# Kernel tuning notes

Hardware: AMD Instinct MI355X
Metric: run time of the kernel (lower is better)

Reference implementation:

```python
import jax, jax.numpy as jnp
import numpy as np

N_NODES = 50000
N_EDGES = 1600000
N_GRAPHS = 64
DIM_IN, DIM_H, HEADS, DIM_OUT = 128, 32, 2, 64
NEG_SLOPE = 0.2


def _segment_softmax(scores, seg, num_segments):
    # scores: [E, H], seg: [E] int -> softmax over edges sharing the same dst
    m = jax.ops.segment_max(scores, seg, num_segments=num_segments)
    m = jnp.where(jnp.isfinite(m), m, 0.0)  # empty segments -> -inf; neutralize
    e = jnp.exp(scores - m[seg])
    s = jax.ops.segment_sum(e, seg, num_segments=num_segments)
    return e / (s[seg] + 1e-16)


def gatv2_conv(x, edge_index, Wl, Wr, att, bias, heads, ch, n_nodes):
    # PyG GATv2Conv defaults: add_self_loops=True, share_weights=False, concat heads.
    loops = jnp.arange(n_nodes, dtype=edge_index.dtype)
    ei = jnp.concatenate([edge_index, jnp.stack([loops, loops])], axis=1)
    src, dst = ei[0], ei[1]
    xl = (x @ Wl).reshape(n_nodes, heads, ch)  # source transform
    xr = (x @ Wr).reshape(n_nodes, heads, ch)  # target transform
    el = xl[src]                               # [E+N, H, C] gather
    s = jax.nn.leaky_relu(el + xr[dst], NEG_SLOPE)
    scores = jnp.einsum('ehc,hc->eh', s, att)  # [E+N, H]
    alpha = _segment_softmax(scores, dst, n_nodes)
    out = jax.ops.segment_sum(alpha[..., None] * el, dst, num_segments=n_nodes)
    return out.reshape(n_nodes, heads * ch) + bias


def setup_inputs() -> dict:
    key = jax.random.key(0)
    ks = jax.random.split(key, 12)
    glorot = lambda k, shp: jax.random.normal(k, shp, jnp.float32) * np.sqrt(2.0 / (shp[0] + shp[-1]))
    x = jax.random.normal(ks[0], (N_NODES, DIM_IN), jnp.float32)
    edge_index = jax.random.randint(ks[1], (2, N_EDGES), 0, N_NODES, jnp.int64)
    batch = jnp.sort(jax.random.randint(ks[2], (N_NODES,), 0, N_GRAPHS, jnp.int64))
    H1 = DIM_H * HEADS
    return {
        'x': x, 'edge_index': edge_index, 'batch': batch,
        'Wl1': glorot(ks[3], (DIM_IN, H1)), 'Wr1': glorot(ks[4], (DIM_IN, H1)),
        'att1': glorot(ks[5], (HEADS, DIM_H)), 'b1': jnp.zeros((H1,), jnp.float32),
        'Wl2': glorot(ks[6], (H1, DIM_OUT)), 'Wr2': glorot(ks[7], (H1, DIM_OUT)),
        'att2': glorot(ks[8], (1, DIM_OUT)), 'b2': jnp.zeros((DIM_OUT,), jnp.float32),
        'lin_w': glorot(ks[9], (DIM_OUT, 2)), 'lin_b': jnp.zeros((2,), jnp.float32),
    }


def reference(x, edge_index, batch, Wl1, Wr1, att1, b1, Wl2, Wr2, att2, b2, lin_w, lin_b):
    # eval mode: dropout is identity
    h = gatv2_conv(x, edge_index, Wl1, Wr1, att1, b1, HEADS, DIM_H, N_NODES)
    h = jax.nn.elu(h)
    h = jax.nn.elu(gatv2_conv(h, edge_index, Wl2, Wr2, att2, b2, 1, DIM_OUT, N_NODES))
    # global mean pool over graphs
    sums = jax.ops.segment_sum(h, batch, num_segments=N_GRAPHS)
    cnts = jax.ops.segment_sum(jnp.ones((N_NODES,), h.dtype), batch, num_segments=N_GRAPHS)
    pooled = sums / jnp.maximum(cnts, 1.0)[:, None]
    return pooled @ lin_w + lin_b
```

## Files before the change

kernel.cpp:

```cpp
#include <hip/hip_runtime.h>
#include <hip/hip_bf16.h>
#include <math.h>

#define N_NODES 50000
#define N_EDGES 1600000
#define N_GRAPHS 64
#define NB 391
#define NBLK 256
#define CHUNK 6250
#define ROW_STRIDE 80
#define SENT 50047

typedef unsigned int u32;

__device__ __forceinline__ float bcf(u32 u) { return __builtin_bit_cast(float, u); }

template <int CTRL>
__device__ __forceinline__ float dpp_add(float v) {
    int r = __builtin_amdgcn_update_dpp(0, __builtin_bit_cast(int, v), CTRL, 0xF, 0xF, true);
    return v + __builtin_bit_cast(float, r);
}

__device__ __forceinline__ u32 pack_bf16x2(float lo, float hi) {
    unsigned short l = __builtin_bit_cast(unsigned short, __float2bfloat16(lo));
    unsigned short h = __builtin_bit_cast(unsigned short, __float2bfloat16(hi));
    return (u32)l | ((u32)h << 16);
}

__global__ __launch_bounds__(256) void count_kernel(
    const int* __restrict__ ei, int* __restrict__ countsRM) {
    __shared__ int h[NB];
    const int t = threadIdx.x;
    for (int k = t; k < NB; k += 256) h[k] = 0;
    __syncthreads();
    const int base = blockIdx.x * CHUNK;
    for (int e = base + t; e < base + CHUNK; e += 256)
        atomicAdd(&h[ei[N_EDGES + e] >> 7], 1);
    __syncthreads();
    for (int k = t; k < NB; k += 256) countsRM[blockIdx.x * NB + k] = h[k];
}

__global__ __launch_bounds__(256) void scan_bucket(
    const int* __restrict__ countsRM, int* __restrict__ scanT,
    int* __restrict__ totals) {
    __shared__ int tmp[256];
    const int b = blockIdx.x;
    const int t = threadIdx.x;
    const int v0 = countsRM[t * NB + b];
    tmp[t] = v0;
    __syncthreads();
    for (int off = 1; off < 256; off <<= 1) {
        int v = (t >= off) ? tmp[t - off] : 0;
        __syncthreads();
        tmp[t] += v;
        __syncthreads();
    }
    scanT[b * 256 + t] = tmp[t] - v0;
    if (t == 255) totals[b] = tmp[t];
}

__global__ __launch_bounds__(512) void scan_total(
    const int* __restrict__ totals, int* __restrict__ bucketBase,
    float* __restrict__ alb) {
    __shared__ int tmp[512];
    const int t = threadIdx.x;
    const int v0 = (t < NB) ? totals[t] : 0;
    tmp[t] = v0;
    __syncthreads();
    for (int off = 1; off < 512; off <<= 1) {
        int v = (t >= off) ? tmp[t - off] : 0;
        __syncthreads();
        tmp[t] += v;
        __syncthreads();
    }
    if (t < NB) bucketBase[t] = tmp[t] - v0;
    if (t == NB - 1) bucketBase[NB] = tmp[t];
    if (t == 0) { alb[(size_t)SENT * 2] = -1e30f; alb[(size_t)SENT * 2 + 1] = -1e30f; }
}

template <int K, bool FUSE_SCATTER>
__global__ __launch_bounds__(256) void gemm_tiled(
    const float* __restrict__ x, const float* __restrict__ Wl,
    const float* __restrict__ Wr, const float* __restrict__ att,
    u32* __restrict__ xlb, float* __restrict__ xr,
    float* __restrict__ alb, float* __restrict__ arb,
    const int* __restrict__ ei, const int* __restrict__ scanT,
    const int* __restrict__ bb, int* __restrict__ sortedE, int gemmBlocks) {
    __shared__ float xs[64][65];
    __shared__ float als[64];
    const int t = threadIdx.x;
    if (FUSE_SCATTER && blockIdx.x >= gemmBlocks) {
        int* cursor = (int*)&xs[0][0];
        const int b = blockIdx.x - gemmBlocks;
        for (int k = t; k < NB; k += 256)
            cursor[k] = bb[k] + scanT[k * 256 + b];
        __syncthreads();
        const int base = b * CHUNK;
        for (int e = base + t; e < base + CHUNK; e += 256) {
            const int s = ei[e];
            const int d = ei[N_EDGES + e];
            const int idx = atomicAdd(&cursor[d >> 7], 1);
            sortedE[idx] = (s << 7) | (d & 127);
        }
        return;
    }
    const int base = blockIdx.x * 64;
    const int lane = t & 63;
    const int w = __builtin_amdgcn_readfirstlane(t >> 6);
    const float* __restrict__ W = (w < 2) ? Wl : Wr;
    const int cb = (w & 1) * 32;
    float acc[32];
#pragma unroll
    for (int j = 0; j < 32; ++j) acc[j] = 0.f;
#pragma unroll
    for (int c = 0; c < K / 64; ++c) {
        if (c) __syncthreads();
        for (int f = t; f < 1024; f += 256) {
            const int row = f >> 4;
            const int c4 = f & 15;
            float4 v = make_float4(0.f, 0.f, 0.f, 0.f);
            if (base + row < N_NODES)
                v = *(const float4*)(x + (size_t)(base + row) * K + c * 64 + c4 * 4);
            xs[row][c4 * 4 + 0] = v.x;
            xs[row][c4 * 4 + 1] = v.y;
            xs[row][c4 * 4 + 2] = v.z;
            xs[row][c4 * 4 + 3] = v.w;
        }
        __syncthreads();
#pragma unroll 2
        for (int kk = 0; kk < 64; ++kk) {
            const float xv = xs[lane][kk];
            const float* __restrict__ Wrow = W + (c * 64 + kk) * 64 + cb;
#pragma unroll
            for (int j = 0; j < 32; ++j) acc[j] = fmaf(xv, Wrow[j], acc[j]);
        }
    }
    const int n = base + lane;
    float av = 0.f;
#pragma unroll
    for (int j = 0; j < 32; ++j) av = fmaf(att[cb + j], acc[j], av);
    if (K == 64) {
        if (w == 0) als[lane] = av;
        __syncthreads();
        if (w == 1 && n < N_NODES) alb[n] = als[lane] + av;
        if (blockIdx.x == 0 && t == 0) alb[SENT] = -1e30f;
    } else {
        if (w < 2 && n < N_NODES) alb[(size_t)n * 2 + (w & 1)] = av;
    }
    if (n < N_NODES) {
        if (w < 2) {
            u32 pk[16];
#pragma unroll
            for (int j = 0; j < 32; j += 2) pk[j >> 1] = pack_bf16x2(acc[j], acc[j + 1]);
            uint4* dst = (uint4*)(xlb + (size_t)n * 32 + (w & 1) * 16);
#pragma unroll
            for (int j = 0; j < 4; ++j)
                dst[j] = make_uint4(pk[j * 4], pk[j * 4 + 1], pk[j * 4 + 2], pk[j * 4 + 3]);
        } else {
            arb[(size_t)n * 2 + (w & 1)] = av;
#pragma unroll
            for (int j = 0; j < 32; j += 4) {
                float4 v = {acc[j], acc[j + 1], acc[j + 2], acc[j + 3]};
                *(float4*)(xr + (size_t)n * 64 + cb + j) = v;
            }
        }
    }
}

__global__ __launch_bounds__(256) void expand_kernel(
    const int* __restrict__ bucketBase, const int* __restrict__ sortedE,
    int* __restrict__ deg, int* __restrict__ rows) {
    __shared__ int ldeg[128];
    const int b = blockIdx.x;
    const int t = threadIdx.x;
    const int node_base = b * 128;
    if (t < 128) {
        const int n = node_base + t;
        ldeg[t] = 1;
        if (n < N_NODES) rows[(size_t)n * ROW_STRIDE] = n;
    }
    __syncthreads();
    const int beg = bucketBase[b];
    const int end = bucketBase[b + 1];
    for (int i = beg + t; i < end; i += 256) {
        const int en = sortedE[i];
        const int ld = en & 127;
        const int pos = atomicAdd(&ldeg[ld], 1);
        if (pos < ROW_STRIDE) rows[(size_t)(node_base + ld) * ROW_STRIDE + pos] = en >> 7;
    }
    __syncthreads();
    if (t < 128) {
        const int n = node_base + t;
        if (n < N_NODES) {
            int c = ldeg[t];
            c = c < ROW_STRIDE ? c : ROW_STRIDE;
            const int cp = (c + 7) & ~7;
            for (int j = c; j < cp; ++j) rows[(size_t)n * ROW_STRIDE + j] = SENT;
            deg[n] = cp;
        }
    }
}

template <bool L1>
__global__ __launch_bounds__(256) void node_layer(
    const int* __restrict__ deg, const int* __restrict__ rows,
    const u32* __restrict__ xlb, const float* __restrict__ xr,
    const float* __restrict__ alb, const float* __restrict__ arb,
    const float* __restrict__ att, const float* __restrict__ bias,
    float* __restrict__ hout) {
    const int n = (blockIdx.x * 256 + threadIdx.x) >> 6;
    const int lane = threadIdx.x & 63;
    const int sub = lane & 7;
    const int g = lane >> 3;
    const float4 xra = *(const float4*)(xr + (size_t)n * 64 + sub * 8);
    const float4 xrb = *(const float4*)(xr + (size_t)n * 64 + sub * 8 + 4);
    const float4 ata = *(const float4*)(att + sub * 8);
    const float4 atb = *(const float4*)(att + sub * 8 + 4);
    const float2 ar2 = *(const float2*)(arb + (size_t)n * 2);
    const float based = 0.6f * (L1 ? ((sub & 4) ? ar2.y : ar2.x) : (ar2.x + ar2.y));

    float c0 = 0.f, c1 = 0.f, c2 = 0.f, c3 = 0.f;
    float c4 = 0.f, c5 = 0.f, c6 = 0.f, c7 = 0.f;
    float ssum = 0.f;
    const int cp = __builtin_amdgcn_readfirstlane(deg[n]);
    const int* __restrict__ row = rows + (size_t)n * ROW_STRIDE;
    for (int i = 0; i < cp; i += 8) {
        const int s = row[i + g];
        const float als = L1 ? alb[(size_t)s * 2 + ((sub >> 2) & 1)] : alb[s];
        const uint4 r4 = *(const uint4*)(xlb + (size_t)s * 32 + sub * 4);
        const float a0 = bcf(r4.x << 16), a1 = bcf(r4.x & 0xFFFF0000u);
        const float a2f = bcf(r4.y << 16), a3 = bcf(r4.y & 0xFFFF0000u);
        const float a4 = bcf(r4.z << 16), a5 = bcf(r4.z & 0xFFFF0000u);
        const float a6 = bcf(r4.w << 16), a7 = bcf(r4.w & 0xFFFF0000u);
        float v = ata.x * fabsf(a0 + xra.x);
        v = fmaf(ata.y, fabsf(a1 + xra.y), v);
        v = fmaf(ata.z, fabsf(a2f + xra.z), v);
        v = fmaf(ata.w, fabsf(a3 + xra.w), v);
        v = fmaf(atb.x, fabsf(a4 + xrb.x), v);
        v = fmaf(atb.y, fabsf(a5 + xrb.y), v);
        v = fmaf(atb.z, fabsf(a6 + xrb.z), v);
        v = fmaf(atb.w, fabsf(a7 + xrb.w), v);
        v = dpp_add<0xB1>(v);
        v = dpp_add<0x4E>(v);
        if (!L1) v = dpp_add<0x141>(v);
        const float ev = __expf(fmaf(0.6f, als, fmaf(0.4f, v, based)));
        c0 = fmaf(ev, a0, c0); c1 = fmaf(ev, a1, c1);
        c2 = fmaf(ev, a2f, c2); c3 = fmaf(ev, a3, c3);
        c4 = fmaf(ev, a4, c4); c5 = fmaf(ev, a5, c5);
        c6 = fmaf(ev, a6, c6); c7 = fmaf(ev, a7, c7);
        ssum += ev;
    }
#define XRED(x) x += __shfl_xor(x, 8); x += __shfl_xor(x, 16); x += __shfl_xor(x, 32);
    XRED(c0) XRED(c1) XRED(c2) XRED(c3) XRED(c4) XRED(c5) XRED(c6) XRED(c7) XRED(ssum)
#undef XRED
    if (g == 0) {
        const float inv = 1.f / (ssum + 1e-16f);
        const float4 ba = *(const float4*)(bias + sub * 8);
        const float4 bb = *(const float4*)(bias + sub * 8 + 4);
        float o[8] = {c0 * inv + ba.x, c1 * inv + ba.y, c2 * inv + ba.z, c3 * inv + ba.w,
                      c4 * inv + bb.x, c5 * inv + bb.y, c6 * inv + bb.z, c7 * inv + bb.w};
#pragma unroll
        for (int j = 0; j < 8; ++j) o[j] = o[j] > 0.f ? o[j] : expm1f(o[j]);
        *(float4*)(hout + (size_t)n * 64 + sub * 8) = make_float4(o[0], o[1], o[2], o[3]);
        *(float4*)(hout + (size_t)n * 64 + sub * 8 + 4) = make_float4(o[4], o[5], o[6], o[7]);
    }
}

__global__ __launch_bounds__(64) void pool_kernel(
    const float* __restrict__ h2, const int* __restrict__ batch,
    float* __restrict__ pooled, float* __restrict__ cnt) {
    const int t = threadIdx.x;
    const int base = blockIdx.x * 64;
    float local = 0.f, lc = 0.f;
    int cur = -1;
    for (int j = 0; j < 64; ++j) {
        const int n = base + j;
        if (n >= N_NODES) break;
        const int g = batch[n];
        if (g != cur) {
            if (cur >= 0) {
                unsafeAtomicAdd(&pooled[cur * 64 + t], local);
                if (t == 0) unsafeAtomicAdd(&cnt[cur], lc);
            }
            cur = g; local = 0.f; lc = 0.f;
        }
        local += h2[n * 64 + t];
        lc += 1.f;
    }
    if (cur >= 0) {
        unsafeAtomicAdd(&pooled[cur * 64 + t], local);
        if (t == 0) unsafeAtomicAdd(&cnt[cur], lc);
    }
}

__global__ __launch_bounds__(128) void head_kernel(
    const float* __restrict__ pooled, const float* __restrict__ cnt,
    const float* __restrict__ lin_w, const float* __restrict__ lin_b,
    float* __restrict__ out) {
    const int i = threadIdx.x;
    const int g = i >> 1, k = i & 1;
    float c = cnt[g];
    c = c > 1.f ? c : 1.f;
    float a = 0.f;
#pragma unroll
    for (int j = 0; j < 64; ++j) a = fmaf(pooled[g * 64 + j] / c, lin_w[j * 2 + k], a);
    out[i] = a + lin_b[k];
}

extern "C" void kernel_launch(void* const* d_in, const int* in_sizes, int n_in,
                              void* d_out, int out_size, void* d_ws, size_t ws_size,
                              hipStream_t stream) {
    const float* x     = (const float*)d_in[0];
    const int*   ei    = (const int*)d_in[1];
    const int*   batch = (const int*)d_in[2];
    const float* Wl1   = (const float*)d_in[3];
    const float* Wr1   = (const float*)d_in[4];
    const float* att1  = (const float*)d_in[5];
    const float* b1    = (const float*)d_in[6];
    const float* Wl2   = (const float*)d_in[7];
    const float* Wr2   = (const float*)d_in[8];
    const float* att2  = (const float*)d_in[9];
    const float* b2    = (const float*)d_in[10];
    const float* lin_w = (const float*)d_in[11];
    const float* lin_b = (const float*)d_in[12];

    float* ws = (float*)d_ws;
    u32*   xlb      = (u32*)ws;
    float* xr       = ws + 1601536;
    float* h1       = ws + 4801536;
    float* alb      = ws + 8001536;
    float* arb      = ws + 8101632;
    int*   rows     = (int*)(ws + 8201728);
    int*   deg      = (int*)(ws + 12205568);
    int*   countsRM = (int*)(ws + 12255616);
    int*   scanT    = (int*)(ws + 12355712);
    int*   totals   = (int*)(ws + 12455808);
    int*   bb       = (int*)(ws + 12456320);
    float* pooled   = ws + 12456832;
    float* cnt      = ws + 12460928;
    int*   sortedE  = (int*)(ws + 12460992);

    hipMemsetAsync(pooled, 0, (size_t)(4096 + 64) * sizeof(float), stream);

    const int gblocks = (N_NODES + 63) / 64;

    count_kernel<<<NBLK, 256, 0, stream>>>(ei, countsRM);
    scan_bucket<<<NB, 256, 0, stream>>>(countsRM, scanT, totals);
    scan_total<<<1, 512, 0, stream>>>(totals, bb, alb);

    gemm_tiled<128, true><<<gblocks + NBLK, 256, 0, stream>>>(
        x, Wl1, Wr1, att1, xlb, xr, alb, arb, ei, scanT, bb, sortedE, gblocks);

    expand_kernel<<<NB, 256, 0, stream>>>(bb, sortedE, deg, rows);

    node_layer<true><<<N_NODES / 4, 256, 0, stream>>>(
        deg, rows, xlb, xr, alb, arb, att1, b1, h1);

    gemm_tiled<64, false><<<gblocks, 256, 0, stream>>>(
        h1, Wl2, Wr2, att2, xlb, xr, alb, arb, nullptr, nullptr, nullptr, nullptr, gblocks);
    node_layer<false><<<N_NODES / 4, 256, 0, stream>>>(
        deg, rows, xlb, xr, alb, arb, att2, b2, h1);

    pool_kernel<<<(N_NODES + 63) / 64, 64, 0, stream>>>(h1, batch, pooled, cnt);
    head_kernel<<<1, 128, 0, stream>>>(pooled, cnt, lin_w, lin_b, (float*)d_out);
}
```

Baseline: 302.8 us.

## Replace scalar FMA GEMMs with bf16 MFMA using split hi/lo weights

Both node-transform GEMMs now use 16x16x32 bf16 MFMA instructions instead of per-thread scalar FMAs. Inputs are pre-converted to bf16 (x in a kernel fused with edge counting, h1 written directly as bf16 by layer 1). Weights are packed into MFMA fragment layout as hi plus lo bf16 parts to keep accuracy close to fp32 on the weight side. The output goes through a shared-memory transpose so the attention dot products and stores can be computed per node. This adds small conversion kernels and introduces bf16 rounding of the activations.

Measured after the change: 297.8 us. Within noise of the previous version (-1.6%).

```diff
diff --git a/kernel.cpp b/kernel.cpp
--- a/kernel.cpp
+++ b/kernel.cpp
@@ -12,6 +12,8 @@
 #define SENT 50047
 
 typedef unsigned int u32;
+typedef __attribute__((ext_vector_type(8))) __bf16 bf16x8;
+typedef __attribute__((ext_vector_type(4))) float f32x4;
 
 __device__ __forceinline__ float bcf(u32 u) { return __builtin_bit_cast(float, u); }
 
@@ -27,17 +29,61 @@
     return (u32)l | ((u32)h << 16);
 }
 
-__global__ __launch_bounds__(256) void count_kernel(
-    const int* __restrict__ ei, int* __restrict__ countsRM) {
+template <int K>
+__global__ __launch_bounds__(256) void conv_w(
+    const float* __restrict__ Wl, const float* __restrict__ Wr,
+    u32* __restrict__ wfHi, u32* __restrict__ wfLo) {
+    const int KO = K / 32;
+    for (int idx = threadIdx.x; idx < KO * 8 * 64; idx += 256) {
+        const int L = idx & 63;
+        const int tile = idx >> 6;
+        const int ko = tile >> 3, nt = tile & 7;
+        const int c = nt * 16 + (L & 15);
+        u32 hi[4], lo[4];
+        float hv[8], lv[8];
+#pragma unroll
+        for (int i = 0; i < 8; ++i) {
+            const int k = ko * 32 + (L >> 4) * 8 + i;
+            const float wv = (c < 64) ? Wl[k * 64 + c] : Wr[k * 64 + (c - 64)];
+            const __hip_bfloat16 h = __float2bfloat16(wv);
+            hv[i] = wv;
+            lv[i] = wv - __bfloat162float(h);
+        }
+#pragma unroll
+        for (int i = 0; i < 4; ++i) {
+            hi[i] = pack_bf16x2(hv[2 * i], hv[2 * i + 1]);
+            lo[i] = pack_bf16x2(lv[2 * i], lv[2 * i + 1]);
+        }
+        *(uint4*)(wfHi + (size_t)idx * 4) = make_uint4(hi[0], hi[1], hi[2], hi[3]);
+        *(uint4*)(wfLo + (size_t)idx * 4) = make_uint4(lo[0], lo[1], lo[2], lo[3]);
+    }
+}
+
+__global__ __launch_bounds__(256) void conv_x_count(
+    const float* __restrict__ x, u32* __restrict__ xbf,
+    const int* __restrict__ ei, int* __restrict__ countsRM, int convBlocks) {
     __shared__ int h[NB];
-    const int t = threadIdx.x;
-    for (int k = t; k < NB; k += 256) h[k] = 0;
-    __syncthreads();
-    const int base = blockIdx.x * CHUNK;
-    for (int e = base + t; e < base + CHUNK; e += 256)
-        atomicAdd(&h[ei[N_EDGES + e] >> 7], 1);
-    __syncthreads();
-    for (int k = t; k < NB; k += 256) countsRM[blockIdx.x * NB + k] = h[k];
+    if (blockIdx.x >= convBlocks) {
+        const int t = threadIdx.x;
+        const int cb = blockIdx.x - convBlocks;
+        for (int k = t; k < NB; k += 256) h[k] = 0;
+        __syncthreads();
+        const int base = cb * CHUNK;
+        for (int e = base + t; e < base + CHUNK; e += 256)
+            atomicAdd(&h[ei[N_EDGES + e] >> 7], 1);
+        __syncthreads();
+        for (int k = t; k < NB; k += 256) countsRM[cb * NB + k] = h[k];
+        return;
+    }
+    const int units = N_NODES * 128 / 8;
+    const int stride = convBlocks * 256;
+    for (int u = blockIdx.x * 256 + threadIdx.x; u < units; u += stride) {
+        const float4 a = *(const float4*)(x + (size_t)u * 8);
+        const float4 b = *(const float4*)(x + (size_t)u * 8 + 4);
+        *(uint4*)(xbf + (size_t)u * 4) = make_uint4(
+            pack_bf16x2(a.x, a.y), pack_bf16x2(a.z, a.w),
+            pack_bf16x2(b.x, b.y), pack_bf16x2(b.z, b.w));
+    }
 }
 
 __global__ __launch_bounds__(256) void scan_bucket(
@@ -79,18 +125,18 @@
 }
 
 template <int K, bool FUSE_SCATTER>
-__global__ __launch_bounds__(256) void gemm_tiled(
-    const float* __restrict__ x, const float* __restrict__ Wl,
-    const float* __restrict__ Wr, const float* __restrict__ att,
+__global__ __launch_bounds__(256) void gemm_mfma(
+    const u32* __restrict__ xbf, const u32* __restrict__ wfHi,
+    const u32* __restrict__ wfLo, const float* __restrict__ att,
     u32* __restrict__ xlb, float* __restrict__ xr,
     float* __restrict__ alb, float* __restrict__ arb,
     const int* __restrict__ ei, const int* __restrict__ scanT,
     const int* __restrict__ bb, int* __restrict__ sortedE, int gemmBlocks) {
-    __shared__ float xs[64][65];
-    __shared__ float als[64];
+    __shared__ float Ct[64][129];
+    __shared__ float alq[64][4];
     const int t = threadIdx.x;
     if (FUSE_SCATTER && blockIdx.x >= gemmBlocks) {
-        int* cursor = (int*)&xs[0][0];
+        int* cursor = (int*)&Ct[0][0];
         const int b = blockIdx.x - gemmBlocks;
         for (int k = t; k < NB; k += 256)
             cursor[k] = bb[k] + scanT[k * 256 + b];
@@ -104,67 +150,91 @@
         }
         return;
     }
-    const int base = blockIdx.x * 64;
+    const int KO = K / 32;
     const int lane = t & 63;
     const int w = __builtin_amdgcn_readfirstlane(t >> 6);
-    const float* __restrict__ W = (w < 2) ? Wl : Wr;
-    const int cb = (w & 1) * 32;
-    float acc[32];
-#pragma unroll
-    for (int j = 0; j < 32; ++j) acc[j] = 0.f;
-#pragma unroll
-    for (int c = 0; c < K / 64; ++c) {
-        if (c) __syncthreads();
-        for (int f = t; f < 1024; f += 256) {
-            const int row = f >> 4;
-            const int c4 = f & 15;
-            float4 v = make_float4(0.f, 0.f, 0.f, 0.f);
-            if (base + row < N_NODES)
-                v = *(const float4*)(x + (size_t)(base + row) * K + c * 64 + c4 * 4);
-            xs[row][c4 * 4 + 0] = v.x;
-            xs[row][c4 * 4 + 1] = v.y;
-            xs[row][c4 * 4 + 2] = v.z;
-            xs[row][c4 * 4 + 3] = v.w;
-        }
-        __syncthreads();
-#pragma unroll 2
-        for (int kk = 0; kk < 64; ++kk) {
-            const float xv = xs[lane][kk];
-            const float* __restrict__ Wrow = W + (c * 64 + kk) * 64 + cb;
-#pragma unroll
-            for (int j = 0; j < 32; ++j) acc[j] = fmaf(xv, Wrow[j], acc[j]);
-        }
-    }
-    const int n = base + lane;
+    const int quad = lane >> 4;
+    const int m16 = lane & 15;
+    const int base = blockIdx.x * 64;
+    const int arow = base + w * 16 + m16;
+    const u32* aptr = xbf + ((size_t)arow * K + quad * 8) / 2;
+
+    f32x4 acc[8];
+    const f32x4 zz = {0.f, 0.f, 0.f, 0.f};
+#pragma unroll
+    for (int i = 0; i < 8; ++i) acc[i] = zz;
+
+#pragma unroll
+    for (int ko = 0; ko < KO; ++ko) {
+        const uint4 au = *(const uint4*)(aptr + ko * 16);
+        const bf16x8 af = __builtin_bit_cast(bf16x8, au);
+#pragma unroll
+        for (int nt = 0; nt < 8; ++nt) {
+            const uint4 bh = *(const uint4*)(wfHi + (size_t)((ko * 8 + nt) * 64 + lane) * 4);
+            acc[nt] = __builtin_amdgcn_mfma_f32_16x16x32_bf16(
+                af, __builtin_bit_cast(bf16x8, bh), acc[nt], 0, 0, 0);
+        }
+#pragma unroll
+        for (int nt = 0; nt < 8; ++nt) {
+            const uint4 bl = *(const uint4*)(wfLo + (size_t)((ko * 8 + nt) * 64 + lane) * 4);
+            acc[nt] = __builtin_amdgcn_mfma_f32_16x16x32_bf16(
+                af, __builtin_bit_cast(bf16x8, bl), acc[nt], 0, 0, 0);
+        }
+    }
+#pragma unroll
+    for (int nt = 0; nt < 8; ++nt)
+#pragma unroll
+        for (int r = 0; r < 4; ++r)
+            Ct[w * 16 + quad * 4 + r][nt * 16 + m16] = acc[nt][r];
+    __syncthreads();
+
+    const int node = t & 63;
+    const int q = t >> 6;
+    const int n = base + node;
     float av = 0.f;
-#pragma unroll
-    for (int j = 0; j < 32; ++j) av = fmaf(att[cb + j], acc[j], av);
-    if (K == 64) {
-        if (w == 0) als[lane] = av;
-        __syncthreads();
-        if (w == 1 && n < N_NODES) alb[n] = als[lane] + av;
-        if (blockIdx.x == 0 && t == 0) alb[SENT] = -1e30f;
-    } else {
-        if (w < 2 && n < N_NODES) alb[(size_t)n * 2 + (w & 1)] = av;
-    }
     if (n < N_NODES) {
-        if (w < 2) {
+        if (q < 2) {
             u32 pk[16];
 #pragma unroll
-            for (int j = 0; j < 32; j += 2) pk[j >> 1] = pack_bf16x2(acc[j], acc[j + 1]);
-            uint4* dst = (uint4*)(xlb + (size_t)n * 32 + (w & 1) * 16);
+            for (int j = 0; j < 32; j += 2) {
+                const float v0 = Ct[node][q * 32 + j];
+                const float v1 = Ct[node][q * 32 + j + 1];
+                av = fmaf(att[q * 32 + j], v0, av);
+                av = fmaf(att[q * 32 + j + 1], v1, av);
+                pk[j >> 1] = pack_bf16x2(v0, v1);
+            }
+            uint4* dst = (uint4*)(xlb + (size_t)n * 32 + q * 16);
 #pragma unroll
             for (int j = 0; j < 4; ++j)
                 dst[j] = make_uint4(pk[j * 4], pk[j * 4 + 1], pk[j * 4 + 2], pk[j * 4 + 3]);
         } else {
-            arb[(size_t)n * 2 + (w & 1)] = av;
+            const int cb = (q - 2) * 32;
 #pragma unroll
             for (int j = 0; j < 32; j += 4) {
-                float4 v = {acc[j], acc[j + 1], acc[j + 2], acc[j + 3]};
+                float4 v = {Ct[node][64 + cb + j], Ct[node][64 + cb + j + 1],
+                            Ct[node][64 + cb + j + 2], Ct[node][64 + cb + j + 3]};
+                av = fmaf(att[cb + j], v.x, av);
+                av = fmaf(att[cb + j + 1], v.y, av);
+                av = fmaf(att[cb + j + 2], v.z, av);
+                av = fmaf(att[cb + j + 3], v.w, av);
                 *(float4*)(xr + (size_t)n * 64 + cb + j) = v;
             }
         }
     }
+    alq[node][q] = av;
+    __syncthreads();
+    if (t < 64 && base + t < N_NODES) {
+        const int nn = base + t;
+        if (K == 128) {
+            alb[(size_t)nn * 2] = alq[t][0];
+            alb[(size_t)nn * 2 + 1] = alq[t][1];
+        } else {
+            alb[nn] = alq[t][0] + alq[t][1];
+        }
+        arb[(size_t)nn * 2] = alq[t][2];
+        arb[(size_t)nn * 2 + 1] = alq[t][3];
+    }
+    if (K == 64 && blockIdx.x == 0 && t == 0) alb[SENT] = -1e30f;
 }
 
 __global__ __launch_bounds__(256) void expand_kernel(
@@ -207,7 +277,7 @@
     const u32* __restrict__ xlb, const float* __restrict__ xr,
     const float* __restrict__ alb, const float* __restrict__ arb,
     const float* __restrict__ att, const float* __restrict__ bias,
-    float* __restrict__ hout) {
+    u32* __restrict__ houtB, float* __restrict__ houtF) {
     const int n = (blockIdx.x * 256 + threadIdx.x) >> 6;
     const int lane = threadIdx.x & 63;
     const int sub = lane & 7;
@@ -261,8 +331,14 @@
                       c4 * inv + bb.x, c5 * inv + bb.y, c6 * inv + bb.z, c7 * inv + bb.w};
 #pragma unroll
         for (int j = 0; j < 8; ++j) o[j] = o[j] > 0.f ? o[j] : expm1f(o[j]);
-        *(float4*)(hout + (size_t)n * 64 + sub * 8) = make_float4(o[0], o[1], o[2], o[3]);
-        *(float4*)(hout + (size_t)n * 64 + sub * 8 + 4) = make_float4(o[4], o[5], o[6], o[7]);
+        if (L1) {
+            *(uint4*)(houtB + (size_t)n * 32 + sub * 4) = make_uint4(
+                pack_bf16x2(o[0], o[1]), pack_bf16x2(o[2], o[3]),
+                pack_bf16x2(o[4], o[5]), pack_bf16x2(o[6], o[7]));
+        } else {
+            *(float4*)(houtF + (size_t)n * 64 + sub * 8) = make_float4(o[0], o[1], o[2], o[3]);
+            *(float4*)(houtF + (size_t)n * 64 + sub * 8 + 4) = make_float4(o[4], o[5], o[6], o[7]);
+        }
     }
 }
 
@@ -325,42 +401,52 @@
     const float* lin_b = (const float*)d_in[12];
 
     float* ws = (float*)d_ws;
-    u32*   xlb      = (u32*)ws;
-    float* xr       = ws + 1601536;
-    float* h1       = ws + 4801536;
-    float* alb      = ws + 8001536;
-    float* arb      = ws + 8101632;
-    int*   rows     = (int*)(ws + 8201728);
-    int*   deg      = (int*)(ws + 12205568);
-    int*   countsRM = (int*)(ws + 12255616);
-    int*   scanT    = (int*)(ws + 12355712);
-    int*   totals   = (int*)(ws + 12455808);
-    int*   bb       = (int*)(ws + 12456320);
-    float* pooled   = ws + 12456832;
-    float* cnt      = ws + 12460928;
-    int*   sortedE  = (int*)(ws + 12460992);
+    u32*   xbf      = (u32*)ws;
+    u32*   h1b      = (u32*)(ws + 3203072);
+    u32*   xlb      = (u32*)(ws + 4804608);
+    float* xr       = ws + 6406144;
+    float* h2       = ws + 9609216;
+    float* alb      = ws + 12812288;
+    float* arb      = ws + 12912384;
+    int*   rows     = (int*)(ws + 13012480);
+    int*   deg      = (int*)(ws + 17016320);
+    int*   countsRM = (int*)(ws + 17066368);
+    int*   scanT    = (int*)(ws + 17166464);
+    int*   totals   = (int*)(ws + 17266560);
+    int*   bb       = (int*)(ws + 17267072);
+    float* pooled   = ws + 17267584;
+    float* cnt      = ws + 17271680;
+    int*   sortedE  = (int*)(ws + 17271744);
+    u32*   wf1hi    = (u32*)(ws + 18871744);
+    u32*   wf1lo    = (u32*)(ws + 18879936);
+    u32*   wf2hi    = (u32*)(ws + 18888128);
+    u32*   wf2lo    = (u32*)(ws + 18892224);
 
     hipMemsetAsync(pooled, 0, (size_t)(4096 + 64) * sizeof(float), stream);
 
     const int gblocks = (N_NODES + 63) / 64;
-
-    count_kernel<<<NBLK, 256, 0, stream>>>(ei, countsRM);
+    const int convBlocks = 512;
+
+    conv_w<128><<<1, 256, 0, stream>>>(Wl1, Wr1, wf1hi, wf1lo);
+    conv_w<64><<<1, 256, 0, stream>>>(Wl2, Wr2, wf2hi, wf2lo);
+    conv_x_count<<<convBlocks + NBLK, 256, 0, stream>>>(x, xbf, ei, countsRM, convBlocks);
+
     scan_bucket<<<NB, 256, 0, stream>>>(countsRM, scanT, totals);
     scan_total<<<1, 512, 0, stream>>>(totals, bb, alb);
 
-    gemm_tiled<128, true><<<gblocks + NBLK, 256, 0, stream>>>(
-        x, Wl1, Wr1, att1, xlb, xr, alb, arb, ei, scanT, bb, sortedE, gblocks);
+    gemm_mfma<128, true><<<gblocks + NBLK, 256, 0, stream>>>(
+        xbf, wf1hi, wf1lo, att1, xlb, xr, alb, arb, ei, scanT, bb, sortedE, gblocks);
 
     expand_kernel<<<NB, 256, 0, stream>>>(bb, sortedE, deg, rows);
 
     node_layer<true><<<N_NODES / 4, 256, 0, stream>>>(
-        deg, rows, xlb, xr, alb, arb, att1, b1, h1);
-
-    gemm_tiled<64, false><<<gblocks, 256, 0, stream>>>(
-        h1, Wl2, Wr2, att2, xlb, xr, alb, arb, nullptr, nullptr, nullptr, nullptr, gblocks);
+        deg, rows, xlb, xr, alb, arb, att1, b1, h1b, nullptr);
+
+    gemm_mfma<64, false><<<gblocks, 256, 0, stream>>>(
+        h1b, wf2hi, wf2lo, att2, xlb, xr, alb, arb, nullptr, nullptr, nullptr, nullptr, gblocks);
     node_layer<false><<<N_NODES / 4, 256, 0, stream>>>(
-        deg, rows, xlb, xr, alb, arb, att2, b2, h1);
-
-    pool_kernel<<<(N_NODES + 63) / 64, 64, 0, stream>>>(h1, batch, pooled, cnt);
+        deg, rows, xlb, xr, alb, arb, att2, b2, nullptr, h2);
+
+    pool_kernel<<<(N_NODES + 63) / 64, 64, 0, stream>>>(h2, batch, pooled, cnt);
     head_kernel<<<1, 128, 0, stream>>>(pooled, cnt, lin_w, lin_b, (float*)d_out);
 }
```
